# Optimization experiments

Measured on AMD Instinct MI355X. Metric: run time of the kernel, lower is better.

Reference implementation:

```python
import jax, jax.numpy as jnp
import numpy as np

N_PRIORS = 125
N_CLASSES = 21
BATCH = 16384
THRESHOLD = 0.3
NEG_POS_RATIO = 3
ALPHA = 1.0


def setup_inputs() -> dict:
    key = jax.random.key(0)
    k1, k2, k3, k4, k5, k6, k7, k8 = jax.random.split(key, 8)
    predicted_locs = jax.random.normal(k1, (BATCH, N_PRIORS, 6), dtype=jnp.float32) * 0.1
    predicted_scores = jax.random.normal(k2, (BATCH, N_PRIORS, N_CLASSES), dtype=jnp.float32)
    # target: (N, 1, 8) = [cx, cy, w, h, angle, sin(a), cos(a), label]
    cxcy = jax.random.uniform(k3, (BATCH, 2), minval=0.2, maxval=0.8)
    wh = jax.random.uniform(k4, (BATCH, 2), minval=0.05, maxval=0.3)
    ang = jax.random.uniform(k5, (BATCH, 1), minval=-3.14159, maxval=3.14159)
    labels = jax.random.randint(k6, (BATCH, 1), 1, N_CLASSES).astype(jnp.float32)
    target = jnp.concatenate([cxcy, wh, ang, jnp.sin(ang), jnp.cos(ang), labels], axis=1)[:, None, :]
    # priors in cxcywh
    pc = jax.random.uniform(k7, (N_PRIORS, 2), minval=0.1, maxval=0.9)
    pwh = jax.random.uniform(k8, (N_PRIORS, 2), minval=0.05, maxval=0.4)
    priors_cxcy = jnp.concatenate([pc, pwh], axis=1)
    return {"predicted_locs": predicted_locs, "predicted_scores": predicted_scores,
            "target": target, "priors_cxcy": priors_cxcy}


def _iou_cxcywh(box, priors):
    # box: (4,), priors: (P,4) in (cx,cy,w,h); axis-aligned IoU
    b_lo = box[:2] - box[2:] * 0.5
    b_hi = box[:2] + box[2:] * 0.5
    p_lo = priors[:, :2] - priors[:, 2:] * 0.5
    p_hi = priors[:, :2] + priors[:, 2:] * 0.5
    inter_wh = jnp.clip(jnp.minimum(b_hi, p_hi) - jnp.maximum(b_lo, p_lo), 0.0)
    inter = inter_wh[:, 0] * inter_wh[:, 1]
    area_b = box[2] * box[3]
    area_p = priors[:, 2] * priors[:, 3]
    return inter / (area_b + area_p - inter)


def _cxcy_to_gcxgcy(cxcy, priors):
    # standard SSD encoding: cxcy (...,4) vs priors (P,4)
    g_cxcy = (cxcy[..., :2] - priors[:, :2]) / (priors[:, 2:] / 10.0)
    g_wh = jnp.log(cxcy[..., 2:] / priors[:, 2:]) * 5.0
    return jnp.concatenate([g_cxcy, g_wh], axis=-1)


def reference(predicted_locs, predicted_scores, target, priors_cxcy):
    P = priors_cxcy.shape[0]
    pred_angles = predicted_locs[..., 4:]   # (N,P,2)
    pred_locs = predicted_locs[..., :4]     # (N,P,4)

    def match(t):  # t: (1, 8), single object per image (n_objects = 1)
        box = t[0, :4]
        ov = _iou_cxcywh(box, priors_cxcy)                 # (P,)
        best_prior = jnp.argmax(ov)                        # prior_for_each_object
        ov = ov.at[best_prior].set(1.0)                    # force-match best prior
        label = jnp.where(ov < THRESHOLD, 0, t[0, 7].astype(jnp.int32))  # (P,)
        true_loc = _cxcy_to_gcxgcy(jnp.broadcast_to(box, (P, 4)), priors_cxcy)
        true_ang = jnp.broadcast_to(t[0, 5:7], (P, 2))
        return true_loc, label, true_ang

    true_locs, true_classes, true_angles = jax.vmap(match)(target)

    pos = true_classes != 0                                # (N,P)
    n_pos = pos.sum(axis=1)                                # (N,)
    n_pos_total = n_pos.sum().astype(jnp.float32)
    posf = pos.astype(jnp.float32)

    # smooth L1 (beta=1), mean over positive elements (4 coords each)
    d = pred_locs - true_locs
    sl1 = jnp.where(jnp.abs(d) < 1.0, 0.5 * d * d, jnp.abs(d) - 0.5)
    loc_loss = (sl1 * posf[..., None]).sum() / (n_pos_total * 4.0)

    # MSE over positive angle pairs, scaled by 25
    da = pred_angles - true_angles
    angle_loss = 25.0 * (da * da * posf[..., None]).sum() / (n_pos_total * 2.0)

    # per-prior cross entropy
    lse = jax.nn.logsumexp(predicted_scores, axis=-1)      # (N,P)
    picked = jnp.take_along_axis(predicted_scores, true_classes[..., None], axis=-1)[..., 0]
    conf_all = lse - picked                                # (N,P)

    conf_pos_sum = (conf_all * posf).sum()
    conf_neg = jnp.where(pos, 0.0, conf_all)
    conf_neg_sorted = -jnp.sort(-conf_neg, axis=1)         # descending
    ranks = jnp.arange(P)[None, :]
    hard = ranks < (NEG_POS_RATIO * n_pos)[:, None]
    conf_hard_neg_sum = (conf_neg_sorted * hard.astype(jnp.float32)).sum()
    conf_loss = (conf_hard_neg_sum + conf_pos_sum) / n_pos_total

    total = conf_loss + ALPHA * loc_loss + angle_loss
    return jnp.stack([conf_loss, loc_loss, angle_loss, total])
```

## Files before the change

kernel.cpp:

```cpp
#include <hip/hip_runtime.h>
#include <math.h>

#define NP 125
#define NC 21
#define TPB 256
#define WPB 4
#define THRESH 0.3f

__global__ void __launch_bounds__(TPB) mbloss_main(
    const float* __restrict__ locs, const float* __restrict__ scores,
    const float* __restrict__ target, const float* __restrict__ priors,
    float4* __restrict__ partials, int batch, int totw) {

    __shared__ float s_sc[WPB][NP * NC];

    const int tid  = threadIdx.x;
    const int wave = tid >> 6;
    const int lane = tid & 63;
    float* sc = s_sc[wave];
    const int wgid = blockIdx.x * WPB + wave;

    const int  p1 = lane + 64;
    const bool v1 = (p1 < NP);
    const float4* pr4 = (const float4*)priors;
    float4 P0 = pr4[lane];
    float4 P1 = v1 ? pr4[p1] : make_float4(0.f, 0.f, 1.f, 1.f);

    float acc_conf = 0.f, acc_sl1 = 0.f, acc_ang = 0.f, acc_np = 0.f;

    for (int r = wgid; r < batch; r += totw) {
        const float* srow = scores + (size_t)r * (NP * NC);
#pragma unroll
        for (int it = 0; it < 41; ++it) sc[it * 64 + lane] = srow[it * 64 + lane];
        if (lane == 0) sc[2624] = srow[2624];

        const float* t = target + (size_t)r * 8;
        const float bx = t[0], by = t[1], bw = t[2], bh = t[3];
        const float sa = t[5], ca = t[6];
        const int lblT = (int)t[7];

        float iou0, iou1 = -1.f;
        {
            float iw = fminf(bx + bw * 0.5f, P0.x + P0.z * 0.5f) -
                       fmaxf(bx - bw * 0.5f, P0.x - P0.z * 0.5f);
            float ih = fminf(by + bh * 0.5f, P0.y + P0.w * 0.5f) -
                       fmaxf(by - bh * 0.5f, P0.y - P0.w * 0.5f);
            iw = fmaxf(iw, 0.f); ih = fmaxf(ih, 0.f);
            float inter = iw * ih;
            iou0 = inter / (bw * bh + P0.z * P0.w - inter);
        }
        if (v1) {
            float iw = fminf(bx + bw * 0.5f, P1.x + P1.z * 0.5f) -
                       fmaxf(bx - bw * 0.5f, P1.x - P1.z * 0.5f);
            float ih = fminf(by + bh * 0.5f, P1.y + P1.w * 0.5f) -
                       fmaxf(by - bh * 0.5f, P1.y - P1.w * 0.5f);
            iw = fmaxf(iw, 0.f); ih = fmaxf(ih, 0.f);
            float inter = iw * ih;
            iou1 = inter / (bw * bh + P1.z * P1.w - inter);
        }

        float bv = iou0; int bi = lane;
        if (iou1 > bv) { bv = iou1; bi = p1; }
#pragma unroll
        for (int off = 1; off < 64; off <<= 1) {
            float vo = __shfl_xor(bv, off, 64);
            int   io = __shfl_xor(bi, off, 64);
            if (vo > bv || (vo == bv && io < bi)) { bv = vo; bi = io; }
        }
        const int best = bi;

        const bool pos0 = (lane == best) || (iou0 >= THRESH);
        const bool pos1 = v1 && ((p1 == best) || (iou1 >= THRESH));
        const int npos = __popcll(__ballot(pos0)) + __popcll(__ballot(pos1));
        acc_np += (pos0 ? 1.f : 0.f) + (pos1 ? 1.f : 0.f);

        float conf0, conf1 = 0.f;
        {
            const float* s0 = sc + lane * NC;
            float m = s0[0];
#pragma unroll
            for (int c = 1; c < NC; ++c) m = fmaxf(m, s0[c]);
            float ss = 0.f;
#pragma unroll
            for (int c = 0; c < NC; ++c) ss += expf(s0[c] - m);
            conf0 = (m + logf(ss)) - s0[pos0 ? lblT : 0];
        }
        if (v1) {
            const float* s1 = sc + p1 * NC;
            float m = s1[0];
#pragma unroll
            for (int c = 1; c < NC; ++c) m = fmaxf(m, s1[c]);
            float ss = 0.f;
#pragma unroll
            for (int c = 0; c < NC; ++c) ss += expf(s1[c] - m);
            conf1 = (m + logf(ss)) - s1[pos1 ? lblT : 0];
        }

#define SL1(d) (fabsf(d) < 1.f ? 0.5f * (d) * (d) : fabsf(d) - 0.5f)
        if (pos0) {
            acc_conf += conf0;
            const float* L = locs + (size_t)r * (NP * 6) + lane * 6;
            float g0 = (bx - P0.x) / (P0.z * 0.1f);
            float g1 = (by - P0.y) / (P0.w * 0.1f);
            float g2 = logf(bw / P0.z) * 5.f;
            float g3 = logf(bh / P0.w) * 5.f;
            float d0 = L[0] - g0, d1 = L[1] - g1, d2 = L[2] - g2, d3 = L[3] - g3;
            acc_sl1 += SL1(d0) + SL1(d1) + SL1(d2) + SL1(d3);
            float a0 = L[4] - sa, a1 = L[5] - ca;
            acc_ang += a0 * a0 + a1 * a1;
        }
        if (pos1) {
            acc_conf += conf1;
            const float* L = locs + (size_t)r * (NP * 6) + p1 * 6;
            float g0 = (bx - P1.x) / (P1.z * 0.1f);
            float g1 = (by - P1.y) / (P1.w * 0.1f);
            float g2 = logf(bw / P1.z) * 5.f;
            float g3 = logf(bh / P1.w) * 5.f;
            float d0 = L[0] - g0, d1 = L[1] - g1, d2 = L[2] - g2, d3 = L[3] - g3;
            acc_sl1 += SL1(d0) + SL1(d1) + SL1(d2) + SL1(d3);
            float a0 = L[4] - sa, a1 = L[5] - ca;
            acc_ang += a0 * a0 + a1 * a1;
        }

        float x0 = pos0 ? 0.f : conf0;
        float x1 = v1 ? (pos1 ? 0.f : conf1) : -1.f;
#pragma unroll
        for (int k = 2; k <= 128; k <<= 1) {
#pragma unroll
            for (int j = k >> 1; j >= 1; j >>= 1) {
                if (j == 64) {
                    float a = fmaxf(x0, x1), b = fminf(x0, x1);
                    x0 = a; x1 = b;
                } else {
                    bool lower = (lane & j) == 0;
                    bool d0 = ((lane & k) == 0);
                    bool d1 = (((lane + 64) & k) == 0);
                    float o0 = __shfl_xor(x0, j, 64);
                    float o1 = __shfl_xor(x1, j, 64);
                    x0 = (lower == d0) ? fmaxf(x0, o0) : fminf(x0, o0);
                    x1 = (lower == d1) ? fmaxf(x1, o1) : fminf(x1, o1);
                }
            }
        }

        int kk = 3 * npos; if (kk > NP) kk = NP;
        acc_conf += (lane < kk ? x0 : 0.f) + (lane + 64 < kk ? x1 : 0.f);
    }

#pragma unroll
    for (int off = 1; off < 64; off <<= 1) {
        acc_conf += __shfl_xor(acc_conf, off, 64);
        acc_sl1  += __shfl_xor(acc_sl1,  off, 64);
        acc_ang  += __shfl_xor(acc_ang,  off, 64);
        acc_np   += __shfl_xor(acc_np,   off, 64);
    }
    if (lane == 0) partials[wgid] = make_float4(acc_conf, acc_sl1, acc_ang, acc_np);
}

__global__ void __launch_bounds__(256) mbloss_fin(const float4* __restrict__ partials,
                                                  int n, float* __restrict__ out) {
    __shared__ float4 red[256];
    const int tid = threadIdx.x;
    float4 a = make_float4(0.f, 0.f, 0.f, 0.f);
    for (int i = tid; i < n; i += 256) {
        float4 p = partials[i];
        a.x += p.x; a.y += p.y; a.z += p.z; a.w += p.w;
    }
    red[tid] = a;
    __syncthreads();
    for (int s = 128; s > 0; s >>= 1) {
        if (tid < s) {
            red[tid].x += red[tid + s].x; red[tid].y += red[tid + s].y;
            red[tid].z += red[tid + s].z; red[tid].w += red[tid + s].w;
        }
        __syncthreads();
    }
    if (tid == 0) {
        float npt  = red[0].w;
        float conf = red[0].x / npt;
        float loc  = red[0].y / (npt * 4.f);
        float ang  = 25.f * red[0].z / (npt * 2.f);
        out[0] = conf; out[1] = loc; out[2] = ang; out[3] = conf + loc + ang;
    }
}

extern "C" void kernel_launch(void* const* d_in, const int* in_sizes, int n_in,
                              void* d_out, int out_size, void* d_ws, size_t ws_size,
                              hipStream_t stream) {
    const float* locs   = (const float*)d_in[0];
    const float* scores = (const float*)d_in[1];
    const float* target = (const float*)d_in[2];
    const float* priors = (const float*)d_in[3];
    float* out = (float*)d_out;

    const int batch = in_sizes[2] / 8;

    int nblk = 2048;
    int max_waves = (int)(ws_size / sizeof(float4));
    if (nblk * WPB > max_waves) nblk = max_waves / WPB;
    if (nblk < 1) nblk = 1;
    const int totw = nblk * WPB;

    float4* partials = (float4*)d_ws;

    mbloss_main<<<nblk, TPB, 0, stream>>>(locs, scores, target, priors,
                                          partials, batch, totw);
    mbloss_fin<<<1, 256, 0, stream>>>(partials, totw, out);
}
```

Baseline: 283.4 us.

## Use async global-to-LDS loads with one image per wave and no grid-stride loop

Replaces the per-lane register-staged copy of scores into shared memory with 16-byte global_load_lds transfers covering four rows per block. The IoU, matching and localization work is done before a barrier so it can overlap the in-flight LDS fill. The grid-stride loop becomes one row per wave with batch/4 blocks, which produces many more partials for the final reduction and assumes the batch is a multiple of 4 and the workspace is large enough. Fast-math __expf/__logf replace the precise versions, with slightly lower accuracy.

```diff
diff --git a/kernel.cpp b/kernel.cpp
--- a/kernel.cpp
+++ b/kernel.cpp
@@ -5,20 +5,45 @@
 #define NC 21
 #define TPB 256
 #define WPB 4
+#define ROWF (NP * NC)
+#define GRPF (WPB * ROWF)
 #define THRESH 0.3f
+
+__device__ inline void ald16(const float* g, float* l) {
+    __builtin_amdgcn_global_load_lds(
+        (const __attribute__((address_space(1))) void*)g,
+        (__attribute__((address_space(3))) void*)l, 16, 0, 0);
+}
 
 __global__ void __launch_bounds__(TPB) mbloss_main(
     const float* __restrict__ locs, const float* __restrict__ scores,
     const float* __restrict__ target, const float* __restrict__ priors,
-    float4* __restrict__ partials, int batch, int totw) {
-
-    __shared__ float s_sc[WPB][NP * NC];
+    float4* __restrict__ partials) {
+
+    __shared__ float s_sc[GRPF];
 
     const int tid  = threadIdx.x;
     const int wave = tid >> 6;
     const int lane = tid & 63;
-    float* sc = s_sc[wave];
-    const int wgid = blockIdx.x * WPB + wave;
+    const int grp  = blockIdx.x;
+    const int r    = grp * WPB + wave;
+
+    const float* gsc = scores + (size_t)grp * GRPF;
+#pragma unroll
+    for (int it = 0; it < 10; ++it) {
+        const int off = it * 1024 + wave * 256 + lane * 4;
+        ald16(gsc + off, s_sc + off);
+    }
+    if (wave == 0) {
+        const int off = 10240 + lane * 4;
+        ald16(gsc + off, s_sc + off);
+    }
+    if (tid < 4) s_sc[10496 + tid] = gsc[10496 + tid];
+
+    const float* t = target + (size_t)r * 8;
+    const float bx = t[0], by = t[1], bw = t[2], bh = t[3];
+    const float sa = t[5], ca = t[6];
+    const int lblT = (int)t[7];
 
     const int  p1 = lane + 64;
     const bool v1 = (p1 < NP);
@@ -26,135 +51,126 @@
     float4 P0 = pr4[lane];
     float4 P1 = v1 ? pr4[p1] : make_float4(0.f, 0.f, 1.f, 1.f);
 
-    float acc_conf = 0.f, acc_sl1 = 0.f, acc_ang = 0.f, acc_np = 0.f;
-
-    for (int r = wgid; r < batch; r += totw) {
-        const float* srow = scores + (size_t)r * (NP * NC);
-#pragma unroll
-        for (int it = 0; it < 41; ++it) sc[it * 64 + lane] = srow[it * 64 + lane];
-        if (lane == 0) sc[2624] = srow[2624];
-
-        const float* t = target + (size_t)r * 8;
-        const float bx = t[0], by = t[1], bw = t[2], bh = t[3];
-        const float sa = t[5], ca = t[6];
-        const int lblT = (int)t[7];
-
-        float iou0, iou1 = -1.f;
-        {
-            float iw = fminf(bx + bw * 0.5f, P0.x + P0.z * 0.5f) -
-                       fmaxf(bx - bw * 0.5f, P0.x - P0.z * 0.5f);
-            float ih = fminf(by + bh * 0.5f, P0.y + P0.w * 0.5f) -
-                       fmaxf(by - bh * 0.5f, P0.y - P0.w * 0.5f);
-            iw = fmaxf(iw, 0.f); ih = fmaxf(ih, 0.f);
-            float inter = iw * ih;
-            iou0 = inter / (bw * bh + P0.z * P0.w - inter);
-        }
-        if (v1) {
-            float iw = fminf(bx + bw * 0.5f, P1.x + P1.z * 0.5f) -
-                       fmaxf(bx - bw * 0.5f, P1.x - P1.z * 0.5f);
-            float ih = fminf(by + bh * 0.5f, P1.y + P1.w * 0.5f) -
-                       fmaxf(by - bh * 0.5f, P1.y - P1.w * 0.5f);
-            iw = fmaxf(iw, 0.f); ih = fmaxf(ih, 0.f);
-            float inter = iw * ih;
-            iou1 = inter / (bw * bh + P1.z * P1.w - inter);
-        }
-
-        float bv = iou0; int bi = lane;
-        if (iou1 > bv) { bv = iou1; bi = p1; }
-#pragma unroll
-        for (int off = 1; off < 64; off <<= 1) {
-            float vo = __shfl_xor(bv, off, 64);
-            int   io = __shfl_xor(bi, off, 64);
-            if (vo > bv || (vo == bv && io < bi)) { bv = vo; bi = io; }
-        }
-        const int best = bi;
-
-        const bool pos0 = (lane == best) || (iou0 >= THRESH);
-        const bool pos1 = v1 && ((p1 == best) || (iou1 >= THRESH));
-        const int npos = __popcll(__ballot(pos0)) + __popcll(__ballot(pos1));
-        acc_np += (pos0 ? 1.f : 0.f) + (pos1 ? 1.f : 0.f);
-
-        float conf0, conf1 = 0.f;
-        {
-            const float* s0 = sc + lane * NC;
-            float m = s0[0];
-#pragma unroll
-            for (int c = 1; c < NC; ++c) m = fmaxf(m, s0[c]);
-            float ss = 0.f;
-#pragma unroll
-            for (int c = 0; c < NC; ++c) ss += expf(s0[c] - m);
-            conf0 = (m + logf(ss)) - s0[pos0 ? lblT : 0];
-        }
-        if (v1) {
-            const float* s1 = sc + p1 * NC;
-            float m = s1[0];
-#pragma unroll
-            for (int c = 1; c < NC; ++c) m = fmaxf(m, s1[c]);
-            float ss = 0.f;
-#pragma unroll
-            for (int c = 0; c < NC; ++c) ss += expf(s1[c] - m);
-            conf1 = (m + logf(ss)) - s1[pos1 ? lblT : 0];
-        }
+    float iou0, iou1 = -1.f;
+    {
+        float iw = fminf(bx + bw * 0.5f, P0.x + P0.z * 0.5f) -
+                   fmaxf(bx - bw * 0.5f, P0.x - P0.z * 0.5f);
+        float ih = fminf(by + bh * 0.5f, P0.y + P0.w * 0.5f) -
+                   fmaxf(by - bh * 0.5f, P0.y - P0.w * 0.5f);
+        iw = fmaxf(iw, 0.f); ih = fmaxf(ih, 0.f);
+        float inter = iw * ih;
+        iou0 = inter / (bw * bh + P0.z * P0.w - inter);
+    }
+    if (v1) {
+        float iw = fminf(bx + bw * 0.5f, P1.x + P1.z * 0.5f) -
+                   fmaxf(bx - bw * 0.5f, P1.x - P1.z * 0.5f);
+        float ih = fminf(by + bh * 0.5f, P1.y + P1.w * 0.5f) -
+                   fmaxf(by - bh * 0.5f, P1.y - P1.w * 0.5f);
+        iw = fmaxf(iw, 0.f); ih = fmaxf(ih, 0.f);
+        float inter = iw * ih;
+        iou1 = inter / (bw * bh + P1.z * P1.w - inter);
+    }
+
+    float bv = iou0; int bi = lane;
+    if (iou1 > bv) { bv = iou1; bi = p1; }
+#pragma unroll
+    for (int off = 1; off < 64; off <<= 1) {
+        float vo = __shfl_xor(bv, off, 64);
+        int   io = __shfl_xor(bi, off, 64);
+        if (vo > bv || (vo == bv && io < bi)) { bv = vo; bi = io; }
+    }
+    const int best = bi;
+
+    const bool pos0 = (lane == best) || (iou0 >= THRESH);
+    const bool pos1 = v1 && ((p1 == best) || (iou1 >= THRESH));
+    const int npos = __popcll(__ballot(pos0)) + __popcll(__ballot(pos1));
+    float acc_conf = 0.f, acc_sl1 = 0.f, acc_ang = 0.f;
+    const float acc_np = (pos0 ? 1.f : 0.f) + (pos1 ? 1.f : 0.f);
 
 #define SL1(d) (fabsf(d) < 1.f ? 0.5f * (d) * (d) : fabsf(d) - 0.5f)
-        if (pos0) {
-            acc_conf += conf0;
-            const float* L = locs + (size_t)r * (NP * 6) + lane * 6;
-            float g0 = (bx - P0.x) / (P0.z * 0.1f);
-            float g1 = (by - P0.y) / (P0.w * 0.1f);
-            float g2 = logf(bw / P0.z) * 5.f;
-            float g3 = logf(bh / P0.w) * 5.f;
-            float d0 = L[0] - g0, d1 = L[1] - g1, d2 = L[2] - g2, d3 = L[3] - g3;
-            acc_sl1 += SL1(d0) + SL1(d1) + SL1(d2) + SL1(d3);
-            float a0 = L[4] - sa, a1 = L[5] - ca;
-            acc_ang += a0 * a0 + a1 * a1;
-        }
-        if (pos1) {
-            acc_conf += conf1;
-            const float* L = locs + (size_t)r * (NP * 6) + p1 * 6;
-            float g0 = (bx - P1.x) / (P1.z * 0.1f);
-            float g1 = (by - P1.y) / (P1.w * 0.1f);
-            float g2 = logf(bw / P1.z) * 5.f;
-            float g3 = logf(bh / P1.w) * 5.f;
-            float d0 = L[0] - g0, d1 = L[1] - g1, d2 = L[2] - g2, d3 = L[3] - g3;
-            acc_sl1 += SL1(d0) + SL1(d1) + SL1(d2) + SL1(d3);
-            float a0 = L[4] - sa, a1 = L[5] - ca;
-            acc_ang += a0 * a0 + a1 * a1;
-        }
-
-        float x0 = pos0 ? 0.f : conf0;
-        float x1 = v1 ? (pos1 ? 0.f : conf1) : -1.f;
-#pragma unroll
-        for (int k = 2; k <= 128; k <<= 1) {
-#pragma unroll
-            for (int j = k >> 1; j >= 1; j >>= 1) {
-                if (j == 64) {
-                    float a = fmaxf(x0, x1), b = fminf(x0, x1);
-                    x0 = a; x1 = b;
-                } else {
-                    bool lower = (lane & j) == 0;
-                    bool d0 = ((lane & k) == 0);
-                    bool d1 = (((lane + 64) & k) == 0);
-                    float o0 = __shfl_xor(x0, j, 64);
-                    float o1 = __shfl_xor(x1, j, 64);
-                    x0 = (lower == d0) ? fmaxf(x0, o0) : fminf(x0, o0);
-                    x1 = (lower == d1) ? fmaxf(x1, o1) : fminf(x1, o1);
-                }
+    if (pos0) {
+        const float* L = locs + (size_t)r * (NP * 6) + lane * 6;
+        float g0 = (bx - P0.x) / (P0.z * 0.1f);
+        float g1 = (by - P0.y) / (P0.w * 0.1f);
+        float g2 = __logf(bw / P0.z) * 5.f;
+        float g3 = __logf(bh / P0.w) * 5.f;
+        float d0 = L[0] - g0, d1 = L[1] - g1, d2 = L[2] - g2, d3 = L[3] - g3;
+        acc_sl1 += SL1(d0) + SL1(d1) + SL1(d2) + SL1(d3);
+        float a0 = L[4] - sa, a1 = L[5] - ca;
+        acc_ang += a0 * a0 + a1 * a1;
+    }
+    if (pos1) {
+        const float* L = locs + (size_t)r * (NP * 6) + p1 * 6;
+        float g0 = (bx - P1.x) / (P1.z * 0.1f);
+        float g1 = (by - P1.y) / (P1.w * 0.1f);
+        float g2 = __logf(bw / P1.z) * 5.f;
+        float g3 = __logf(bh / P1.w) * 5.f;
+        float d0 = L[0] - g0, d1 = L[1] - g1, d2 = L[2] - g2, d3 = L[3] - g3;
+        acc_sl1 += SL1(d0) + SL1(d1) + SL1(d2) + SL1(d3);
+        float a0 = L[4] - sa, a1 = L[5] - ca;
+        acc_ang += a0 * a0 + a1 * a1;
+    }
+
+    __syncthreads();
+
+    const float* myrow = s_sc + wave * ROWF;
+    float conf0, conf1 = 0.f;
+    {
+        const float* s0 = myrow + lane * NC;
+        float m = s0[0];
+#pragma unroll
+        for (int c = 1; c < NC; ++c) m = fmaxf(m, s0[c]);
+        float ss = 0.f;
+#pragma unroll
+        for (int c = 0; c < NC; ++c) ss += __expf(s0[c] - m);
+        conf0 = (m + __logf(ss)) - s0[pos0 ? lblT : 0];
+    }
+    if (v1) {
+        const float* s1 = myrow + p1 * NC;
+        float m = s1[0];
+#pragma unroll
+        for (int c = 1; c < NC; ++c) m = fmaxf(m, s1[c]);
+        float ss = 0.f;
+#pragma unroll
+        for (int c = 0; c < NC; ++c) ss += __expf(s1[c] - m);
+        conf1 = (m + __logf(ss)) - s1[pos1 ? lblT : 0];
+    }
+    if (pos0) acc_conf += conf0;
+    if (pos1) acc_conf += conf1;
+
+    float x0 = pos0 ? 0.f : conf0;
+    float x1 = v1 ? (pos1 ? 0.f : conf1) : -1.f;
+#pragma unroll
+    for (int k = 2; k <= 128; k <<= 1) {
+#pragma unroll
+        for (int j = k >> 1; j >= 1; j >>= 1) {
+            if (j == 64) {
+                float a = fmaxf(x0, x1), b = fminf(x0, x1);
+                x0 = a; x1 = b;
+            } else {
+                bool lower = (lane & j) == 0;
+                bool d0 = ((lane & k) == 0);
+                bool d1 = (((lane + 64) & k) == 0);
+                float o0 = __shfl_xor(x0, j, 64);
+                float o1 = __shfl_xor(x1, j, 64);
+                x0 = (lower == d0) ? fmaxf(x0, o0) : fminf(x0, o0);
+                x1 = (lower == d1) ? fmaxf(x1, o1) : fminf(x1, o1);
             }
         }
-
-        int kk = 3 * npos; if (kk > NP) kk = NP;
-        acc_conf += (lane < kk ? x0 : 0.f) + (lane + 64 < kk ? x1 : 0.f);
-    }
-
+    }
+
+    int kk = 3 * npos; if (kk > NP) kk = NP;
+    acc_conf += (lane < kk ? x0 : 0.f) + (lane + 64 < kk ? x1 : 0.f);
+
+    float rc = acc_conf, rs = acc_sl1, ra = acc_ang, rn = acc_np;
 #pragma unroll
     for (int off = 1; off < 64; off <<= 1) {
-        acc_conf += __shfl_xor(acc_conf, off, 64);
-        acc_sl1  += __shfl_xor(acc_sl1,  off, 64);
-        acc_ang  += __shfl_xor(acc_ang,  off, 64);
-        acc_np   += __shfl_xor(acc_np,   off, 64);
-    }
-    if (lane == 0) partials[wgid] = make_float4(acc_conf, acc_sl1, acc_ang, acc_np);
+        rc += __shfl_xor(rc, off, 64);
+        rs += __shfl_xor(rs, off, 64);
+        ra += __shfl_xor(ra, off, 64);
+        rn += __shfl_xor(rn, off, 64);
+    }
+    if (lane == 0) partials[r] = make_float4(rc, rs, ra, rn);
 }
 
 __global__ void __launch_bounds__(256) mbloss_fin(const float4* __restrict__ partials,
@@ -194,16 +210,10 @@
     float* out = (float*)d_out;
 
     const int batch = in_sizes[2] / 8;
-
-    int nblk = 2048;
-    int max_waves = (int)(ws_size / sizeof(float4));
-    if (nblk * WPB > max_waves) nblk = max_waves / WPB;
-    if (nblk < 1) nblk = 1;
-    const int totw = nblk * WPB;
+    const int nblk  = batch / WPB;
 
     float4* partials = (float4*)d_ws;
 
-    mbloss_main<<<nblk, TPB, 0, stream>>>(locs, scores, target, priors,
-                                          partials, batch, totw);
-    mbloss_fin<<<1, 256, 0, stream>>>(partials, totw, out);
-}
+    mbloss_main<<<nblk, TPB, 0, stream>>>(locs, scores, target, priors, partials);
+    mbloss_fin<<<1, 256, 0, stream>>>(partials, batch, out);
+}
```

Result: no change. 286.3 us (+1.0%).
